# Kernel tuning notes

Measured on AMD Instinct MI355X. Metric: run time of the kernel, lower is better.

The kernel has to match this reference:

```python
import jax, jax.numpy as jnp
import numpy as np

N_NODES = 100000
N_EDGES = 1600000
IN_C, HID_C, OUT_C = 128, 128, 64
DROPOUT_P = 0.5


def setup_inputs() -> dict:
    key = jax.random.key(0)
    ks = jax.random.split(key, 12)
    x = jax.random.normal(ks[0], (N_NODES, IN_C), dtype=jnp.float32)
    edge_index = jax.random.randint(ks[1], (2, N_EDGES), 0, N_NODES, dtype=jnp.int64)
    # Glorot-ish init scale for linear weights
    def w(k, fi, fo):
        return jax.random.normal(k, (fi, fo), dtype=jnp.float32) * (1.0 / np.sqrt(fi))
    return {
        "x": x,
        "edge_index": edge_index,
        "Wl0": w(ks[2], IN_C, HID_C), "Wr0": w(ks[3], IN_C, HID_C), "b0": jnp.zeros((HID_C,), jnp.float32),
        "Wl1": w(ks[4], HID_C, HID_C), "Wr1": w(ks[5], HID_C, HID_C), "b1": jnp.zeros((HID_C,), jnp.float32),
        "Wl2": w(ks[6], HID_C, OUT_C), "Wr2": w(ks[7], HID_C, OUT_C), "b2": jnp.zeros((OUT_C,), jnp.float32),
    }


def _sage_conv(x, src, dst, Wl, Wr, b):
    # mean-aggregate neighbor features x[src] at dst, then two linears + bias
    n = x.shape[0]
    agg = jax.ops.segment_sum(x[src], dst, num_segments=n)          # [N, d]
    cnt = jax.ops.segment_sum(jnp.ones((src.shape[0],), x.dtype), dst, num_segments=n)
    mean = agg / jnp.maximum(cnt, 1.0)[:, None]
    return mean @ Wl + x @ Wr + b


def _dropout(x, key, p):
    keep = jax.random.bernoulli(key, 1.0 - p, x.shape)
    return jnp.where(keep, x / (1.0 - p), 0.0).astype(x.dtype)


def reference(x, edge_index, Wl0, Wr0, b0, Wl1, Wr1, b1, Wl2, Wr2, b2):
    src, dst = edge_index[0], edge_index[1]
    dk = jax.random.split(jax.random.key(42), 2)
    h = _sage_conv(x, src, dst, Wl0, Wr0, b0)
    h = _dropout(jax.nn.relu(h), dk[0], DROPOUT_P)
    h = _sage_conv(h, src, dst, Wl1, Wr1, b1)
    h = _dropout(jax.nn.relu(h), dk[1], DROPOUT_P)
    h = _sage_conv(h, src, dst, Wl2, Wr2, b2)
    return h
```

## Files before the change

### kernel.cpp

```cpp
#include <hip/hip_runtime.h>
#include <stdint.h>

typedef __attribute__((ext_vector_type(8))) short s8v;
typedef __attribute__((ext_vector_type(4))) float f4v;

constexpr int ECHUNK = 4096;

__host__ __device__ inline uint32_t rotl32(uint32_t x, int r) {
    return (x << r) | (x >> (32 - r));
}

__host__ __device__ inline void tf2x32(uint32_t k0, uint32_t k1,
                                       uint32_t x0, uint32_t x1,
                                       uint32_t& o0, uint32_t& o1) {
    const uint32_t ks0 = k0, ks1 = k1, ks2 = k0 ^ k1 ^ 0x1BD11BDAu;
    x0 += ks0; x1 += ks1;
    x0 += x1; x1 = rotl32(x1, 13); x1 ^= x0;
    x0 += x1; x1 = rotl32(x1, 15); x1 ^= x0;
    x0 += x1; x1 = rotl32(x1, 26); x1 ^= x0;
    x0 += x1; x1 = rotl32(x1, 6);  x1 ^= x0;
    x0 += ks1; x1 += ks2 + 1u;
    x0 += x1; x1 = rotl32(x1, 17); x1 ^= x0;
    x0 += x1; x1 = rotl32(x1, 29); x1 ^= x0;
    x0 += x1; x1 = rotl32(x1, 16); x1 ^= x0;
    x0 += x1; x1 = rotl32(x1, 24); x1 ^= x0;
    x0 += ks2; x1 += ks0 + 2u;
    x0 += x1; x1 = rotl32(x1, 13); x1 ^= x0;
    x0 += x1; x1 = rotl32(x1, 15); x1 ^= x0;
    x0 += x1; x1 = rotl32(x1, 26); x1 ^= x0;
    x0 += x1; x1 = rotl32(x1, 6);  x1 ^= x0;
    x0 += ks0; x1 += ks1 + 3u;
    x0 += x1; x1 = rotl32(x1, 17); x1 ^= x0;
    x0 += x1; x1 = rotl32(x1, 29); x1 ^= x0;
    x0 += x1; x1 = rotl32(x1, 16); x1 ^= x0;
    x0 += x1; x1 = rotl32(x1, 24); x1 ^= x0;
    x0 += ks1; x1 += ks2 + 4u;
    x0 += x1; x1 = rotl32(x1, 13); x1 ^= x0;
    x0 += x1; x1 = rotl32(x1, 15); x1 ^= x0;
    x0 += x1; x1 = rotl32(x1, 26); x1 ^= x0;
    x0 += x1; x1 = rotl32(x1, 6);  x1 ^= x0;
    x0 += ks2; x1 += ks0 + 5u;
    o0 = x0; o1 = x1;
}

__device__ inline bool tf_keep(uint32_t idx, uint32_t k0, uint32_t k1) {
    uint32_t o0, o1;
    tf2x32(k0, k1, 0u, idx, o0, o1);
    return ((o0 ^ o1) >> 31) == 0u;
}

__device__ inline uint16_t f2bf(float f) {
    uint32_t u = __float_as_uint(f);
    return (uint16_t)((u + 0x7fffu + ((u >> 16) & 1u)) >> 16);
}
__device__ inline float bflo(uint32_t v) { return __uint_as_float(v << 16); }
__device__ inline float bfhi(uint32_t v) { return __uint_as_float(v & 0xffff0000u); }

__global__ void detect_kernel(const int* __restrict__ w, int* __restrict__ flag64) {
    __shared__ int s[256];
    int t = threadIdx.x;
    int acc = 0;
    for (int i = t; i < 2048; i += 256) acc |= w[2 * i + 1];
    s[t] = acc;
    __syncthreads();
    for (int off = 128; off > 0; off >>= 1) {
        if (t < off) s[t] |= s[t + off];
        __syncthreads();
    }
    if (t == 0) *flag64 = (s[0] == 0) ? 1 : 0;
}

__device__ inline int edge_src(const int* w, int e, int f64) {
    return f64 ? w[2 * e] : w[e];
}
__device__ inline int edge_dst(const int* w, int e, int E, int f64) {
    return f64 ? w[2 * E + 2 * e] : w[E + e];
}


__global__ __launch_bounds__(256) void bucketcount_kernel(
        const int* __restrict__ w, const int* __restrict__ flag64,
        int* __restrict__ hist, int E, int nA, int NBUK) {
    __shared__ int cnt[256];
    int t = threadIdx.x;
    if (t < NBUK) cnt[t] = 0;
    __syncthreads();
    int f64 = *flag64;
    int lo = blockIdx.x * ECHUNK, hi = min(E, lo + ECHUNK);
    for (int e = lo + t; e < hi; e += 256)
        atomicAdd(&cnt[edge_dst(w, e, E, f64) >> 9], 1);
    __syncthreads();
    if (t < NBUK) hist[t * nA + blockIdx.x] = cnt[t];
}

__global__ void scan1_kernel(const int* __restrict__ in, int* __restrict__ out,
                             int* __restrict__ bsum, int n) {
    __shared__ int s[512];
    int t = threadIdx.x;
    int i = blockIdx.x * 512 + t;
    int v = (i < n) ? in[i] : 0;
    s[t] = v;
    __syncthreads();
    for (int off = 1; off < 512; off <<= 1) {
        int x = (t >= off) ? s[t - off] : 0;
        __syncthreads();
        s[t] += x;
        __syncthreads();
    }
    if (i < n) out[i + 1] = s[t];
    if (t == 511) bsum[blockIdx.x] = s[511];
}

__global__ void scan2_kernel(int* __restrict__ bsum, int nb) {
    if (threadIdx.x == 0 && blockIdx.x == 0) {
        int run = 0;
        for (int b = 0; b < nb; ++b) { int tmp = bsum[b]; bsum[b] = run; run += tmp; }
    }
}

__global__ void scan3_kernel(int* __restrict__ out, const int* __restrict__ bsum, int n) {
    int i = blockIdx.x * 512 + threadIdx.x;
    if (i < n) out[i + 1] += bsum[blockIdx.x];
    if (i == 0) out[0] = 0;
}

__global__ __launch_bounds__(256) void bucketscatter_kernel(
        const int* __restrict__ w, const int* __restrict__ flag64,
        const int* __restrict__ bofs, uint2* __restrict__ tmp, int E, int nA, int NBUK) {
    __shared__ int sbase[256];
    int t = threadIdx.x;
    if (t < NBUK) sbase[t] = bofs[t * nA + blockIdx.x];
    __syncthreads();
    int f64 = *flag64;
    int lo = blockIdx.x * ECHUNK, hi = min(E, lo + ECHUNK);
    for (int e = lo + t; e < hi; e += 256) {
        int s = edge_src(w, e, f64);
        int d = edge_dst(w, e, E, f64);
        int p = atomicAdd(&sbase[d >> 9], 1);
        tmp[p] = make_uint2((unsigned)s, (unsigned)d);
    }
}

__global__ __launch_bounds__(256) void bucketdeg_kernel(
        const uint2* __restrict__ tmp, const int* __restrict__ bofs,
        int* __restrict__ deg, int nA, int N) {
    __shared__ int cnt[512];
    int b = blockIdx.x;
    int node0 = b << 9;
    int nn = min(512, N - node0);
    int t = threadIdx.x;
    for (int i = t; i < nn; i += 256) cnt[i] = 0;
    __syncthreads();
    int lo = bofs[b * nA], hi = bofs[(b + 1) * nA];
    for (int e = lo + t; e < hi; e += 256)
        atomicAdd(&cnt[(int)tmp[e].y - node0], 1);
    __syncthreads();
    for (int i = t; i < nn; i += 256) deg[node0 + i] = cnt[i];
}

__global__ __launch_bounds__(256) void finescatter_kernel(
        const uint2* __restrict__ tmp, const int* __restrict__ bofs,
        const int* __restrict__ rowptr, int* __restrict__ col, int nA, int N) {
    __shared__ int cur[512];
    int b = blockIdx.x;
    int node0 = b << 9;
    int nn = min(512, N - node0);
    int t = threadIdx.x;
    for (int i = t; i < nn; i += 256) cur[i] = rowptr[node0 + i];
    __syncthreads();
    int lo = bofs[b * nA], hi = bofs[(b + 1) * nA];
    for (int e = lo + t; e < hi; e += 256) {
        uint2 p = tmp[e];
        int q = atomicAdd(&cur[(int)p.y - node0], 1);
        col[q] = (int)p.x;
    }
}

__global__ void convx_kernel(const float* __restrict__ in, uint16_t* __restrict__ out, int n4) {
    int i = blockIdx.x * blockDim.x + threadIdx.x;
    if (i >= n4) return;
    float4 v = *(const float4*)(in + (size_t)i * 4);
    uint16_t o[4] = { f2bf(v.x), f2bf(v.y), f2bf(v.z), f2bf(v.w) };
    *(uint2*)(out + (size_t)i * 4) = *(uint2*)o;
}

__global__ void convw_kernel(const float* __restrict__ W, uint16_t* __restrict__ Wt, int N) {
    int i = blockIdx.x * blockDim.x + threadIdx.x;
    if (i >= N * 128) return;
    int n = i >> 7, k = i & 127;
    Wt[i] = f2bf(W[(size_t)k * N + n]);
}

__global__ __launch_bounds__(256) void pair_gemm_kernel(
        const uint16_t* __restrict__ Xb, const uint16_t* __restrict__ WtL,
        const uint16_t* __restrict__ WtR, const float* __restrict__ bias,
        uint16_t* __restrict__ YL, float* __restrict__ Z, int M, int N) {
    const int l   = threadIdx.x & 63;
    const int wv  = threadIdx.x >> 6;
    const int row0 = blockIdx.x * 64 + wv * 16;
    const int ml  = l & 15;
    const int kg  = l >> 4;

    int arow = row0 + ml; if (arow >= M) arow = M - 1;
    const uint16_t* xr = Xb + (size_t)arow * 128 + kg * 8;
    s8v a0 = *(const s8v*)(xr);
    s8v a1 = *(const s8v*)(xr + 32);
    s8v a2 = *(const s8v*)(xr + 64);
    s8v a3 = *(const s8v*)(xr + 96);

    const int drow = row0 + kg * 4;

    for (int n0 = 0; n0 < N; n0 += 16) {
        const uint16_t* wl = WtL + (size_t)(n0 + ml) * 128 + kg * 8;
        const uint16_t* wr = WtR + (size_t)(n0 + ml) * 128 + kg * 8;
        f4v accL = {0.f, 0.f, 0.f, 0.f};
        f4v accR = {0.f, 0.f, 0.f, 0.f};
        accL = __builtin_amdgcn_mfma_f32_16x16x32_bf16(a0, *(const s8v*)(wl), accL, 0, 0, 0);
        accR = __builtin_amdgcn_mfma_f32_16x16x32_bf16(a0, *(const s8v*)(wr), accR, 0, 0, 0);
        accL = __builtin_amdgcn_mfma_f32_16x16x32_bf16(a1, *(const s8v*)(wl + 32), accL, 0, 0, 0);
        accR = __builtin_amdgcn_mfma_f32_16x16x32_bf16(a1, *(const s8v*)(wr + 32), accR, 0, 0, 0);
        accL = __builtin_amdgcn_mfma_f32_16x16x32_bf16(a2, *(const s8v*)(wl + 64), accL, 0, 0, 0);
        accR = __builtin_amdgcn_mfma_f32_16x16x32_bf16(a2, *(const s8v*)(wr + 64), accR, 0, 0, 0);
        accL = __builtin_amdgcn_mfma_f32_16x16x32_bf16(a3, *(const s8v*)(wl + 96), accL, 0, 0, 0);
        accR = __builtin_amdgcn_mfma_f32_16x16x32_bf16(a3, *(const s8v*)(wr + 96), accR, 0, 0, 0);

        float bv = bias[n0 + ml];
#pragma unroll
        for (int r = 0; r < 4; ++r) {
            int g = drow + r;
            if (g < M) {
                YL[(size_t)g * N + n0 + ml] = f2bf(accL[r]);
                Z [(size_t)g * N + n0 + ml] = accR[r] + bv;
            }
        }
    }
}

__global__ __launch_bounds__(256) void agg128_kernel(
        const uint16_t* __restrict__ Yl, const float* __restrict__ Z,
        const int* __restrict__ rowptr, const int* __restrict__ col,
        uint16_t* __restrict__ H, int n, uint32_t k0, uint32_t k1) {
    int node = blockIdx.x * 4 + (threadIdx.x >> 6);
    if (node >= n) return;
    int lane = threadIdx.x & 63;
    const uint32_t* ylp = (const uint32_t*)Yl;
    int beg = rowptr[node], end = rowptr[node + 1];
    float ax = 0.f, ay = 0.f;
    int e = beg;
    for (; e + 3 < end; e += 4) {
        int j0 = col[e], j1 = col[e + 1], j2 = col[e + 2], j3 = col[e + 3];
        uint32_t v0 = ylp[(size_t)j0 * 64 + lane];
        uint32_t v1 = ylp[(size_t)j1 * 64 + lane];
        uint32_t v2 = ylp[(size_t)j2 * 64 + lane];
        uint32_t v3 = ylp[(size_t)j3 * 64 + lane];
        ax += bflo(v0) + bflo(v1) + bflo(v2) + bflo(v3);
        ay += bfhi(v0) + bfhi(v1) + bfhi(v2) + bfhi(v3);
    }
    for (; e < end; ++e) {
        uint32_t v = ylp[(size_t)col[e] * 64 + lane];
        ax += bflo(v); ay += bfhi(v);
    }
    int cnt = end - beg;
    float inv = 1.0f / (float)(cnt > 1 ? cnt : 1);
    float2 z = *(const float2*)(Z + (size_t)node * 128 + lane * 2);
    float hx = fmaxf(ax * inv + z.x, 0.0f);
    float hy = fmaxf(ay * inv + z.y, 0.0f);
    uint32_t idx = (uint32_t)node * 128u + (uint32_t)lane * 2u;
    hx = tf_keep(idx, k0, k1)      ? hx * 2.0f : 0.0f;
    hy = tf_keep(idx + 1u, k0, k1) ? hy * 2.0f : 0.0f;
    uint32_t packed = (uint32_t)f2bf(hx) | ((uint32_t)f2bf(hy) << 16);
    ((uint32_t*)H)[(size_t)node * 64 + lane] = packed;
}

__global__ __launch_bounds__(256) void agg64_kernel(
        const uint16_t* __restrict__ Yl, const float* __restrict__ Z,
        const int* __restrict__ rowptr, const int* __restrict__ col,
        float* __restrict__ out, int n) {
    int node = blockIdx.x * 4 + (threadIdx.x >> 6);
    if (node >= n) return;
    int lane = threadIdx.x & 63;
    int beg = rowptr[node], end = rowptr[node + 1];
    float a = 0.f;
    int e = beg;
    for (; e + 3 < end; e += 4) {
        int j0 = col[e], j1 = col[e + 1], j2 = col[e + 2], j3 = col[e + 3];
        float v0 = __uint_as_float(((uint32_t)Yl[(size_t)j0 * 64 + lane]) << 16);
        float v1 = __uint_as_float(((uint32_t)Yl[(size_t)j1 * 64 + lane]) << 16);
        float v2 = __uint_as_float(((uint32_t)Yl[(size_t)j2 * 64 + lane]) << 16);
        float v3 = __uint_as_float(((uint32_t)Yl[(size_t)j3 * 64 + lane]) << 16);
        a += v0 + v1 + v2 + v3;
    }
    for (; e < end; ++e)
        a += __uint_as_float(((uint32_t)Yl[(size_t)col[e] * 64 + lane]) << 16);
    int cnt = end - beg;
    float inv = 1.0f / (float)(cnt > 1 ? cnt : 1);
    out[(size_t)node * 64 + lane] = a * inv + Z[(size_t)node * 64 + lane];
}

extern "C" void kernel_launch(void* const* d_in, const int* in_sizes, int n_in,
                              void* d_out, int out_size, void* d_ws, size_t ws_size,
                              hipStream_t stream) {
    const float* x   = (const float*)d_in[0];
    const int*   ei  = (const int*)d_in[1];
    const float* Wl0 = (const float*)d_in[2];
    const float* Wr0 = (const float*)d_in[3];
    const float* b0  = (const float*)d_in[4];
    const float* Wl1 = (const float*)d_in[5];
    const float* Wr1 = (const float*)d_in[6];
    const float* b1  = (const float*)d_in[7];
    const float* Wl2 = (const float*)d_in[8];
    const float* Wr2 = (const float*)d_in[9];
    const float* b2  = (const float*)d_in[10];

    const int N = in_sizes[0] / 128;
    const int E = in_sizes[1] / 2;
    const int* srcp = ei;

    const int nA   = (E + ECHUNK - 1) / ECHUNK;
    const int NBUK = (N + 511) >> 9;
    const int L    = NBUK * nA;

    char* ws = (char*)d_ws;
    size_t off = 0;
    auto alloc = [&](size_t bytes) {
        size_t o = off;
        off = (off + bytes + 255) & ~(size_t)255;
        return o;
    };
    int*      rowptr = (int*)(ws + alloc((size_t)(N + 1) * 4));
    int*      deg    = (int*)(ws + alloc((size_t)N * 4));
    int*      bsum   = (int*)(ws + alloc(1024 * 4));
    int*      flag64 = (int*)(ws + alloc(256));
    int*      hist   = (int*)(ws + alloc((size_t)L * 4));
    int*      bofs   = (int*)(ws + alloc((size_t)(L + 1) * 4));
    uint2*    tmp    = (uint2*)(ws + alloc((size_t)E * 8));
    int*      col    = (int*)(ws + alloc((size_t)E * 4));
    uint16_t* Xb     = (uint16_t*)(ws + alloc((size_t)N * 128 * 2));
    uint16_t* Hb     = (uint16_t*)(ws + alloc((size_t)N * 128 * 2));
    uint16_t* Byl    = (uint16_t*)(ws + alloc((size_t)N * 128 * 2));
    float*    Cz     = (float*)(ws + alloc((size_t)N * 128 * 4));
    uint16_t* Wt0l   = (uint16_t*)(ws + alloc(128 * 128 * 2));
    uint16_t* Wt0r   = (uint16_t*)(ws + alloc(128 * 128 * 2));
    uint16_t* Wt1l   = (uint16_t*)(ws + alloc(128 * 128 * 2));
    uint16_t* Wt1r   = (uint16_t*)(ws + alloc(128 * 128 * 2));
    uint16_t* Wt2l   = (uint16_t*)(ws + alloc(128 * 128 * 2));
    uint16_t* Wt2r   = (uint16_t*)(ws + alloc(128 * 128 * 2));

    uint32_t k00, k01, k10, k11;
    tf2x32(0u, 42u, 0u, 0u, k00, k01);
    tf2x32(0u, 42u, 0u, 1u, k10, k11);

    detect_kernel<<<1, 256, 0, stream>>>(srcp, flag64);
    bucketcount_kernel<<<nA, 256, 0, stream>>>(srcp, flag64, hist, E, nA, NBUK);
    int NBL = (L + 511) / 512;
    scan1_kernel<<<NBL, 512, 0, stream>>>(hist, bofs, bsum, L);
    scan2_kernel<<<1, 64, 0, stream>>>(bsum, NBL);
    scan3_kernel<<<NBL, 512, 0, stream>>>(bofs, bsum, L);
    bucketscatter_kernel<<<nA, 256, 0, stream>>>(srcp, flag64, bofs, tmp, E, nA, NBUK);
    bucketdeg_kernel<<<NBUK, 256, 0, stream>>>(tmp, bofs, deg, nA, N);
    int NBN = (N + 511) / 512;
    scan1_kernel<<<NBN, 512, 0, stream>>>(deg, rowptr, bsum, N);
    scan2_kernel<<<1, 64, 0, stream>>>(bsum, NBN);
    scan3_kernel<<<NBN, 512, 0, stream>>>(rowptr, bsum, N);
    finescatter_kernel<<<NBUK, 256, 0, stream>>>(tmp, bofs, rowptr, col, nA, N);

    convx_kernel<<<(N * 128 / 4 + 255) / 256, 256, 0, stream>>>(x, Xb, N * 128 / 4);
    convw_kernel<<<64, 256, 0, stream>>>(Wl0, Wt0l, 128);
    convw_kernel<<<64, 256, 0, stream>>>(Wr0, Wt0r, 128);
    convw_kernel<<<64, 256, 0, stream>>>(Wl1, Wt1l, 128);
    convw_kernel<<<64, 256, 0, stream>>>(Wr1, Wt1r, 128);
    convw_kernel<<<32, 256, 0, stream>>>(Wl2, Wt2l, 64);
    convw_kernel<<<32, 256, 0, stream>>>(Wr2, Wt2r, 64);

    dim3 blk(256);
    dim3 gg((N + 63) / 64);
    dim3 gagg((N + 3) / 4);

    pair_gemm_kernel<<<gg, blk, 0, stream>>>(Xb, Wt0l, Wt0r, b0, Byl, Cz, N, 128);
    agg128_kernel<<<gagg, blk, 0, stream>>>(Byl, Cz, rowptr, col, Hb, N, k00, k01);
    pair_gemm_kernel<<<gg, blk, 0, stream>>>(Hb, Wt1l, Wt1r, b1, Byl, Cz, N, 128);
    agg128_kernel<<<gagg, blk, 0, stream>>>(Byl, Cz, rowptr, col, Hb, N, k10, k11);
    pair_gemm_kernel<<<gg, blk, 0, stream>>>(Hb, Wt2l, Wt2r, b2, Byl, Cz, N, 64);
    agg64_kernel<<<gagg, blk, 0, stream>>>(Byl, Cz, rowptr, col, (float*)d_out, N);
}
```

Measured before the change: 626.0 us.

## Store root-term in bf16, widen aggregation loads, and merge weight-convert launches

The root-linear output Z is now written and read as bf16 instead of fp32, halving that buffer's traffic. The aggregation kernels map two nodes per wavefront, with each half-wave loading 8 bytes per lane instead of 4, so gathers are wider and fewer lanes sit idle. The six weight-conversion launches are merged into one 2D-grid launch. The risk is extra rounding error from bf16 Z and lower parallelism per node on long neighbor lists.

```diff
diff --git a/kernel.cpp b/kernel.cpp
--- a/kernel.cpp
+++ b/kernel.cpp
@@ -77,7 +77,6 @@
     return f64 ? w[2 * E + 2 * e] : w[E + e];
 }
 
-
 __global__ __launch_bounds__(256) void bucketcount_kernel(
         const int* __restrict__ w, const int* __restrict__ flag64,
         int* __restrict__ hist, int E, int nA, int NBUK) {
@@ -184,17 +183,24 @@
     *(uint2*)(out + (size_t)i * 4) = *(uint2*)o;
 }
 
-__global__ void convw_kernel(const float* __restrict__ W, uint16_t* __restrict__ Wt, int N) {
+struct WPack {
+    const float* src[6];
+    uint16_t*    dst[6];
+    int          n[6];
+};
+__global__ void convw_all_kernel(WPack p) {
+    int s = blockIdx.y;
     int i = blockIdx.x * blockDim.x + threadIdx.x;
-    if (i >= N * 128) return;
-    int n = i >> 7, k = i & 127;
-    Wt[i] = f2bf(W[(size_t)k * N + n]);
+    int total = p.n[s] * 128;
+    if (i >= total) return;
+    int nn = i >> 7, k = i & 127;
+    p.dst[s][i] = f2bf(p.src[s][(size_t)k * p.n[s] + nn]);
 }
 
 __global__ __launch_bounds__(256) void pair_gemm_kernel(
         const uint16_t* __restrict__ Xb, const uint16_t* __restrict__ WtL,
         const uint16_t* __restrict__ WtR, const float* __restrict__ bias,
-        uint16_t* __restrict__ YL, float* __restrict__ Z, int M, int N) {
+        uint16_t* __restrict__ YL, uint16_t* __restrict__ ZB, int M, int N) {
     const int l   = threadIdx.x & 63;
     const int wv  = threadIdx.x >> 6;
     const int row0 = blockIdx.x * 64 + wv * 16;
@@ -230,71 +236,90 @@
             int g = drow + r;
             if (g < M) {
                 YL[(size_t)g * N + n0 + ml] = f2bf(accL[r]);
-                Z [(size_t)g * N + n0 + ml] = accR[r] + bv;
+                ZB[(size_t)g * N + n0 + ml] = f2bf(accR[r] + bv);
             }
         }
     }
 }
 
 __global__ __launch_bounds__(256) void agg128_kernel(
-        const uint16_t* __restrict__ Yl, const float* __restrict__ Z,
+        const uint16_t* __restrict__ Yl, const uint16_t* __restrict__ Zb,
         const int* __restrict__ rowptr, const int* __restrict__ col,
         uint16_t* __restrict__ H, int n, uint32_t k0, uint32_t k1) {
-    int node = blockIdx.x * 4 + (threadIdx.x >> 6);
+    int wv = threadIdx.x >> 6, lane = threadIdx.x & 63;
+    int half = lane >> 5, sl = lane & 31;
+    int node = blockIdx.x * 8 + wv * 2 + half;
     if (node >= n) return;
-    int lane = threadIdx.x & 63;
-    const uint32_t* ylp = (const uint32_t*)Yl;
+    const uint2* ylp = (const uint2*)Yl;
     int beg = rowptr[node], end = rowptr[node + 1];
-    float ax = 0.f, ay = 0.f;
+    float a0 = 0.f, a1 = 0.f, a2 = 0.f, a3 = 0.f;
     int e = beg;
     for (; e + 3 < end; e += 4) {
         int j0 = col[e], j1 = col[e + 1], j2 = col[e + 2], j3 = col[e + 3];
-        uint32_t v0 = ylp[(size_t)j0 * 64 + lane];
-        uint32_t v1 = ylp[(size_t)j1 * 64 + lane];
-        uint32_t v2 = ylp[(size_t)j2 * 64 + lane];
-        uint32_t v3 = ylp[(size_t)j3 * 64 + lane];
-        ax += bflo(v0) + bflo(v1) + bflo(v2) + bflo(v3);
-        ay += bfhi(v0) + bfhi(v1) + bfhi(v2) + bfhi(v3);
+        uint2 v0 = ylp[(size_t)j0 * 32 + sl];
+        uint2 v1 = ylp[(size_t)j1 * 32 + sl];
+        uint2 v2 = ylp[(size_t)j2 * 32 + sl];
+        uint2 v3 = ylp[(size_t)j3 * 32 + sl];
+        a0 += bflo(v0.x) + bflo(v1.x) + bflo(v2.x) + bflo(v3.x);
+        a1 += bfhi(v0.x) + bfhi(v1.x) + bfhi(v2.x) + bfhi(v3.x);
+        a2 += bflo(v0.y) + bflo(v1.y) + bflo(v2.y) + bflo(v3.y);
+        a3 += bfhi(v0.y) + bfhi(v1.y) + bfhi(v2.y) + bfhi(v3.y);
     }
     for (; e < end; ++e) {
-        uint32_t v = ylp[(size_t)col[e] * 64 + lane];
-        ax += bflo(v); ay += bfhi(v);
+        uint2 v = ylp[(size_t)col[e] * 32 + sl];
+        a0 += bflo(v.x); a1 += bfhi(v.x);
+        a2 += bflo(v.y); a3 += bfhi(v.y);
     }
     int cnt = end - beg;
     float inv = 1.0f / (float)(cnt > 1 ? cnt : 1);
-    float2 z = *(const float2*)(Z + (size_t)node * 128 + lane * 2);
-    float hx = fmaxf(ax * inv + z.x, 0.0f);
-    float hy = fmaxf(ay * inv + z.y, 0.0f);
-    uint32_t idx = (uint32_t)node * 128u + (uint32_t)lane * 2u;
-    hx = tf_keep(idx, k0, k1)      ? hx * 2.0f : 0.0f;
-    hy = tf_keep(idx + 1u, k0, k1) ? hy * 2.0f : 0.0f;
-    uint32_t packed = (uint32_t)f2bf(hx) | ((uint32_t)f2bf(hy) << 16);
-    ((uint32_t*)H)[(size_t)node * 64 + lane] = packed;
+    uint2 z = ((const uint2*)Zb)[(size_t)node * 32 + sl];
+    float h0 = fmaxf(a0 * inv + bflo(z.x), 0.0f);
+    float h1 = fmaxf(a1 * inv + bfhi(z.x), 0.0f);
+    float h2 = fmaxf(a2 * inv + bflo(z.y), 0.0f);
+    float h3 = fmaxf(a3 * inv + bfhi(z.y), 0.0f);
+    uint32_t idx = (uint32_t)node * 128u + (uint32_t)sl * 4u;
+    h0 = tf_keep(idx,      k0, k1) ? h0 * 2.0f : 0.0f;
+    h1 = tf_keep(idx + 1u, k0, k1) ? h1 * 2.0f : 0.0f;
+    h2 = tf_keep(idx + 2u, k0, k1) ? h2 * 2.0f : 0.0f;
+    h3 = tf_keep(idx + 3u, k0, k1) ? h3 * 2.0f : 0.0f;
+    uint2 o;
+    o.x = (uint32_t)f2bf(h0) | ((uint32_t)f2bf(h1) << 16);
+    o.y = (uint32_t)f2bf(h2) | ((uint32_t)f2bf(h3) << 16);
+    ((uint2*)H)[(size_t)node * 32 + sl] = o;
 }
 
 __global__ __launch_bounds__(256) void agg64_kernel(
-        const uint16_t* __restrict__ Yl, const float* __restrict__ Z,
+        const uint16_t* __restrict__ Yl, const uint16_t* __restrict__ Zb,
         const int* __restrict__ rowptr, const int* __restrict__ col,
         float* __restrict__ out, int n) {
-    int node = blockIdx.x * 4 + (threadIdx.x >> 6);
+    int wv = threadIdx.x >> 6, lane = threadIdx.x & 63;
+    int half = lane >> 5, sl = lane & 31;
+    int node = blockIdx.x * 8 + wv * 2 + half;
     if (node >= n) return;
-    int lane = threadIdx.x & 63;
+    const uint32_t* ylp = (const uint32_t*)Yl;
     int beg = rowptr[node], end = rowptr[node + 1];
-    float a = 0.f;
+    float a0 = 0.f, a1 = 0.f;
     int e = beg;
     for (; e + 3 < end; e += 4) {
         int j0 = col[e], j1 = col[e + 1], j2 = col[e + 2], j3 = col[e + 3];
-        float v0 = __uint_as_float(((uint32_t)Yl[(size_t)j0 * 64 + lane]) << 16);
-        float v1 = __uint_as_float(((uint32_t)Yl[(size_t)j1 * 64 + lane]) << 16);
-        float v2 = __uint_as_float(((uint32_t)Yl[(size_t)j2 * 64 + lane]) << 16);
-        float v3 = __uint_as_float(((uint32_t)Yl[(size_t)j3 * 64 + lane]) << 16);
-        a += v0 + v1 + v2 + v3;
-    }
-    for (; e < end; ++e)
-        a += __uint_as_float(((uint32_t)Yl[(size_t)col[e] * 64 + lane]) << 16);
+        uint32_t v0 = ylp[(size_t)j0 * 32 + sl];
+        uint32_t v1 = ylp[(size_t)j1 * 32 + sl];
+        uint32_t v2 = ylp[(size_t)j2 * 32 + sl];
+        uint32_t v3 = ylp[(size_t)j3 * 32 + sl];
+        a0 += bflo(v0) + bflo(v1) + bflo(v2) + bflo(v3);
+        a1 += bfhi(v0) + bfhi(v1) + bfhi(v2) + bfhi(v3);
+    }
+    for (; e < end; ++e) {
+        uint32_t v = ylp[(size_t)col[e] * 32 + sl];
+        a0 += bflo(v); a1 += bfhi(v);
+    }
     int cnt = end - beg;
     float inv = 1.0f / (float)(cnt > 1 ? cnt : 1);
-    out[(size_t)node * 64 + lane] = a * inv + Z[(size_t)node * 64 + lane];
+    uint32_t z = ((const uint32_t*)Zb)[(size_t)node * 32 + sl];
+    float2 o;
+    o.x = a0 * inv + bflo(z);
+    o.y = a1 * inv + bfhi(z);
+    *(float2*)(out + (size_t)node * 64 + sl * 2) = o;
 }
 
 extern "C" void kernel_launch(void* const* d_in, const int* in_sizes, int n_in,
@@ -338,7 +363,7 @@
     uint16_t* Xb     = (uint16_t*)(ws + alloc((size_t)N * 128 * 2));
     uint16_t* Hb     = (uint16_t*)(ws + alloc((size_t)N * 128 * 2));
     uint16_t* Byl    = (uint16_t*)(ws + alloc((size_t)N * 128 * 2));
-    float*    Cz     = (float*)(ws + alloc((size_t)N * 128 * 4));
+    uint16_t* Czb    = (uint16_t*)(ws + alloc((size_t)N * 128 * 2));
     uint16_t* Wt0l   = (uint16_t*)(ws + alloc(128 * 128 * 2));
     uint16_t* Wt0r   = (uint16_t*)(ws + alloc(128 * 128 * 2));
     uint16_t* Wt1l   = (uint16_t*)(ws + alloc(128 * 128 * 2));
@@ -365,21 +390,23 @@
     finescatter_kernel<<<NBUK, 256, 0, stream>>>(tmp, bofs, rowptr, col, nA, N);
 
     convx_kernel<<<(N * 128 / 4 + 255) / 256, 256, 0, stream>>>(x, Xb, N * 128 / 4);
-    convw_kernel<<<64, 256, 0, stream>>>(Wl0, Wt0l, 128);
-    convw_kernel<<<64, 256, 0, stream>>>(Wr0, Wt0r, 128);
-    convw_kernel<<<64, 256, 0, stream>>>(Wl1, Wt1l, 128);
-    convw_kernel<<<64, 256, 0, stream>>>(Wr1, Wt1r, 128);
-    convw_kernel<<<32, 256, 0, stream>>>(Wl2, Wt2l, 64);
-    convw_kernel<<<32, 256, 0, stream>>>(Wr2, Wt2r, 64);
+    WPack wp;
+    wp.src[0] = Wl0; wp.dst[0] = Wt0l; wp.n[0] = 128;
+    wp.src[1] = Wr0; wp.dst[1] = Wt0r; wp.n[1] = 128;
+    wp.src[2] = Wl1; wp.dst[2] = Wt1l; wp.n[2] = 128;
+    wp.src[3] = Wr1; wp.dst[3] = Wt1r; wp.n[3] = 128;
+    wp.src[4] = Wl2; wp.dst[4] = Wt2l; wp.n[4] = 64;
+    wp.src[5] = Wr2; wp.dst[5] = Wt2r; wp.n[5] = 64;
+    convw_all_kernel<<<dim3(64, 6), 256, 0, stream>>>(wp);
 
     dim3 blk(256);
     dim3 gg((N + 63) / 64);
-    dim3 gagg((N + 3) / 4);
-
-    pair_gemm_kernel<<<gg, blk, 0, stream>>>(Xb, Wt0l, Wt0r, b0, Byl, Cz, N, 128);
-    agg128_kernel<<<gagg, blk, 0, stream>>>(Byl, Cz, rowptr, col, Hb, N, k00, k01);
-    pair_gemm_kernel<<<gg, blk, 0, stream>>>(Hb, Wt1l, Wt1r, b1, Byl, Cz, N, 128);
-    agg128_kernel<<<gagg, blk, 0, stream>>>(Byl, Cz, rowptr, col, Hb, N, k10, k11);
-    pair_gemm_kernel<<<gg, blk, 0, stream>>>(Hb, Wt2l, Wt2r, b2, Byl, Cz, N, 64);
-    agg64_kernel<<<gagg, blk, 0, stream>>>(Byl, Cz, rowptr, col, (float*)d_out, N);
-}
+    dim3 gagg((N + 7) / 8);
+
+    pair_gemm_kernel<<<gg, blk, 0, stream>>>(Xb, Wt0l, Wt0r, b0, Byl, Czb, N, 128);
+    agg128_kernel<<<gagg, blk, 0, stream>>>(Byl, Czb, rowptr, col, Hb, N, k00, k01);
+    pair_gemm_kernel<<<gg, blk, 0, stream>>>(Hb, Wt1l, Wt1r, b1, Byl, Czb, N, 128);
+    agg128_kernel<<<gagg, blk, 0, stream>>>(Byl, Czb, rowptr, col, Hb, N, k10, k11);
+    pair_gemm_kernel<<<gg, blk, 0, stream>>>(Hb, Wt2l, Wt2r, b2, Byl, Czb, N, 64);
+    agg64_kernel<<<gagg, blk, 0, stream>>>(Byl, Czb, rowptr, col, (float*)d_out, N);
+}
```

Measured after the change: 565.4 us. -9.7%, faster.
